# Optimization experiments

Measured on AMD Instinct MI355X. Metric: run time of the kernel, lower is better.

Reference implementation:

```python
import jax, jax.numpy as jnp
import numpy as np

CHANNELS = 512
NUM_HEADS = 8
NUM_GROUPS = 32
EPS = 1e-5


def setup_inputs() -> dict:
    key = jax.random.key(0)
    ks = jax.random.split(key, 6)
    c = CHANNELS
    x = jax.random.normal(ks[0], (8, c, 32, 32), dtype=jnp.float32)
    norm_w = jnp.ones((c,), jnp.float32)
    norm_b = jnp.zeros((c,), jnp.float32)
    # 1x1 conv1d weights stored as [out, in]
    qkv_w = jax.random.normal(ks[1], (3 * c, c), jnp.float32) * (1.0 / np.sqrt(c))
    qkv_b = jax.random.normal(ks[2], (3 * c,), jnp.float32) * 0.02
    # proj_out is zero-initialized in the original; use small random values so the
    # residual branch is exercised numerically (init values are not part of the math).
    proj_w = jax.random.normal(ks[3], (c, c), jnp.float32) * 0.02
    proj_b = jax.random.normal(ks[4], (c,), jnp.float32) * 0.02
    return {"x": x, "norm_w": norm_w, "norm_b": norm_b,
            "qkv_w": qkv_w, "qkv_b": qkv_b, "proj_w": proj_w, "proj_b": proj_b}


def _group_norm(x, w, b):
    # x: [B, C, L]; normalize per (batch, group) over (C/G, L) in float32
    B, C, L = x.shape
    xg = x.astype(jnp.float32).reshape(B, NUM_GROUPS, (C // NUM_GROUPS) * L)
    mean = xg.mean(axis=-1, keepdims=True)
    var = xg.var(axis=-1, keepdims=True)
    xn = ((xg - mean) * jax.lax.rsqrt(var + EPS)).reshape(B, C, L)
    return (xn * w[None, :, None] + b[None, :, None]).astype(x.dtype)


def _attention_legacy(qkv, n_heads):
    # qkv: [B, 3*C, L]  (QKVAttentionLegacy: split heads after reshape)
    B, width, L = qkv.shape
    ch = width // (3 * n_heads)
    q, k, v = jnp.split(qkv.reshape(B * n_heads, 3 * ch, L), 3, axis=1)
    scale = 1.0 / np.sqrt(np.sqrt(ch))
    w = jnp.einsum('bct,bcs->bts', q * scale, k * scale)  # [B*H, L, L]
    w = jax.nn.softmax(w.astype(jnp.float32), axis=-1).astype(qkv.dtype)
    a = jnp.einsum('bts,bcs->bct', w, v)  # [B*H, ch, L]
    return a.reshape(B, n_heads * ch, L)


def reference(x, norm_w, norm_b, qkv_w, qkv_b, proj_w, proj_b):
    b, c = x.shape[0], x.shape[1]
    spatial = x.shape[2:]
    x_ = x.reshape(b, c, -1)  # [B, C, L]
    xn = _group_norm(x_, norm_w, norm_b)
    qkv = jnp.einsum('oc,bcl->bol', qkv_w, xn) + qkv_b[None, :, None]
    h = _attention_legacy(qkv, NUM_HEADS)
    h = jnp.einsum('oc,bcl->bol', proj_w, h) + proj_b[None, :, None]
    return (x_ + h).reshape(b, c, *spatial)
```

## Files before the change

### kernel.cpp

```cpp
#include <hip/hip_runtime.h>
#include <hip/hip_bf16.h>
#include <stdint.h>


#define NB 8
#define NC 512
#define NL 1024
#define NHD 8
#define ND 64

typedef __attribute__((ext_vector_type(4))) float f32x4;
typedef __attribute__((ext_vector_type(8))) short bf16x8;
typedef __attribute__((ext_vector_type(4))) short bf16x4;
typedef __attribute__((ext_vector_type(4))) unsigned short u16x4;
typedef __attribute__((ext_vector_type(8))) unsigned short u16x8;

#define MFMA16(a, b, c) __builtin_amdgcn_mfma_f32_16x16x32_bf16((a), (b), (c), 0, 0, 0)

static __device__ __forceinline__ f32x4 mfma_k16(bf16x4 a, bf16x4 b, f32x4 c) {
#if __has_builtin(__builtin_amdgcn_mfma_f32_16x16x16bf16_1k)
  return __builtin_amdgcn_mfma_f32_16x16x16bf16_1k(a, b, c, 0, 0, 0);
#else
  asm("v_mfma_f32_16x16x16_bf16 %0, %1, %2, %0" : "+v"(c) : "v"(a), "v"(b));
  return c;
#endif
}

#if __has_builtin(__builtin_amdgcn_exp2f)
#define EXP2F __builtin_amdgcn_exp2f
#else
#define EXP2F exp2f
#endif

static __device__ __forceinline__ unsigned short f2bf(float f) {
  union { float f; uint32_t u; } v; v.f = f;
  uint32_t r = v.u + 0x7fffu + ((v.u >> 16) & 1u);
  return (unsigned short)(r >> 16);
}

static __device__ __forceinline__ short f2bf_h(float f) {
  __hip_bfloat16 h = __float2bfloat16(f);
  return *reinterpret_cast<short*>(&h);
}

static __device__ __forceinline__ void gl_lds16(const unsigned short* g, unsigned short* l) {
  __builtin_amdgcn_global_load_lds(
      (const __attribute__((address_space(1))) void*)g,
      (__attribute__((address_space(3))) void*)l, 16, 0, 0);
}

__global__ __launch_bounds__(256) void k_conv_w(const float* __restrict__ qkvw,
                                                const float* __restrict__ pw,
                                                unsigned short* __restrict__ qwb,
                                                unsigned short* __restrict__ pwb) {
  int i = blockIdx.x * 256 + threadIdx.x;
  const int NQ4 = (3 * NC * NC) / 4;
  if (i < NQ4) {
    f32x4 v = ((const f32x4*)qkvw)[i];
    u16x4 o; o.x = f2bf(v.x); o.y = f2bf(v.y); o.z = f2bf(v.z); o.w = f2bf(v.w);
    ((u16x4*)qwb)[i] = o;
  } else {
    int j = i - NQ4;
    f32x4 v = ((const f32x4*)pw)[j];
    u16x4 o; o.x = f2bf(v.x); o.y = f2bf(v.y); o.z = f2bf(v.z); o.w = f2bf(v.w);
    ((u16x4*)pwb)[j] = o;
  }
}

__global__ __launch_bounds__(256) void k_gnorm(const float* __restrict__ x,
                                               const float* __restrict__ nw,
                                               const float* __restrict__ nb,
                                               unsigned short* __restrict__ xnt) {
  const int b = blockIdx.x >> 5, g = blockIdx.x & 31;
  const float* base = x + ((size_t)b * NC + g * 16) * NL;
  const int t = threadIdx.x;
  f32x4 vals[16];
  float s = 0.f, ss = 0.f;
#pragma unroll
  for (int r = 0; r < 16; ++r) {
    f32x4 v = ((const f32x4*)base)[t + 256 * r];
    vals[r] = v;
    s += v.x + v.y + v.z + v.w;
    ss += v.x * v.x + v.y * v.y + v.z * v.z + v.w * v.w;
  }
#pragma unroll
  for (int m = 1; m < 64; m <<= 1) { s += __shfl_xor(s, m, 64); ss += __shfl_xor(ss, m, 64); }
  __shared__ float red[8];
  const int w = t >> 6;
  if ((t & 63) == 0) { red[w] = s; red[4 + w] = ss; }
  __syncthreads();
  s  = red[0] + red[1] + red[2] + red[3];
  ss = red[4] + red[5] + red[6] + red[7];
  const float mean = s * (1.f / 16384.f);
  const float var  = ss * (1.f / 16384.f) - mean * mean;
  const float inv  = rsqrtf(var + 1e-5f);
  u16x8 ov[4][2];
#pragma unroll
  for (int r = 0; r < 16; ++r) {
    float wcv = nw[g * 16 + r] * inv;
    float bcv = nb[g * 16 + r] - mean * wcv;
    f32x4 v = vals[r];
    ov[0][r >> 3][r & 7] = f2bf(v.x * wcv + bcv);
    ov[1][r >> 3][r & 7] = f2bf(v.y * wcv + bcv);
    ov[2][r >> 3][r & 7] = f2bf(v.z * wcv + bcv);
    ov[3][r >> 3][r & 7] = f2bf(v.w * wcv + bcv);
  }
#pragma unroll
  for (int j = 0; j < 4; ++j) {
    size_t off = ((size_t)b * NL + 4 * t + j) * NC + g * 16;
    *(u16x8*)(xnt + off)     = ov[j][0];
    *(u16x8*)(xnt + off + 8) = ov[j][1];
  }
}

__global__ __launch_bounds__(256) void k_qkv(const unsigned short* __restrict__ xnt,
                                             const unsigned short* __restrict__ qwb,
                                             const float* __restrict__ qkvb,
                                             unsigned short* __restrict__ qt,
                                             unsigned short* __restrict__ kt,
                                             unsigned short* __restrict__ vt) {
  __shared__ __align__(16) unsigned short As[128 * 64];
  __shared__ __align__(16) unsigned short Bs[128 * 64];
  const int m0 = blockIdx.x * 128;
  const int n0 = blockIdx.y * 128;
  const int b = blockIdx.z;
  const int tid = threadIdx.x, lane = tid & 63, w = tid >> 6;
  const int wr = w >> 1, wc = w & 1;

  int soff[4];
#pragma unroll
  for (int r = 0; r < 4; ++r) {
    int c = (r * 4 + w) * 64 + lane;
    int row = c >> 3, lc = (c & 7) ^ (row & 7);
    soff[r] = row * NC + lc * 8;
  }
  const unsigned short* Ap = xnt + (size_t)b * NL * NC + (size_t)m0 * NC;
  const unsigned short* Bp = qwb + (size_t)n0 * NC;

  f32x4 acc[4][4];
#pragma unroll
  for (int mi = 0; mi < 4; ++mi)
#pragma unroll
    for (int ni = 0; ni < 4; ++ni) acc[mi][ni] = (f32x4){0.f, 0.f, 0.f, 0.f};

  for (int k0 = 0; k0 < NC; k0 += 64) {
#pragma unroll
    for (int r = 0; r < 4; ++r) gl_lds16(Ap + soff[r], &As[(r * 4 + w) * 512]);
#pragma unroll
    for (int r = 0; r < 4; ++r) gl_lds16(Bp + soff[r], &Bs[(r * 4 + w) * 512]);
    Ap += 64; Bp += 64;
    __syncthreads();
#pragma unroll
    for (int ks = 0; ks < 2; ++ks) {
      bf16x8 af[4], bfr[4];
#pragma unroll
      for (int mi = 0; mi < 4; ++mi) {
        int row = wr * 64 + mi * 16 + (lane & 15);
        int ph = ((lane >> 4) + ks * 4) ^ (row & 7);
        af[mi] = *(const bf16x8*)&As[row * 64 + ph * 8];
      }
#pragma unroll
      for (int ni = 0; ni < 4; ++ni) {
        int row = wc * 64 + ni * 16 + (lane & 15);
        int ph = ((lane >> 4) + ks * 4) ^ (row & 7);
        bfr[ni] = *(const bf16x8*)&Bs[row * 64 + ph * 8];
      }
#pragma unroll
      for (int mi = 0; mi < 4; ++mi)
#pragma unroll
        for (int ni = 0; ni < 4; ++ni)
          acc[mi][ni] = MFMA16(af[mi], bfr[ni], acc[mi][ni]);
    }
    __syncthreads();
  }
#pragma unroll
  for (int ni = 0; ni < 4; ++ni) {
    int o = n0 + wc * 64 + ni * 16 + (lane & 15);
    int head = o / 192, rem = o - head * 192;
    int type = rem >> 6, ch = rem & 63;
    float bias = qkvb[o];
#pragma unroll
    for (int mi = 0; mi < 4; ++mi) {
      int l0 = m0 + wr * 64 + mi * 16 + ((lane >> 4) << 2);
      if (type == 2) {
        u16x4 pk;
#pragma unroll
        for (int i = 0; i < 4; ++i) pk[i] = f2bf(acc[mi][ni][i] + bias);
        *(u16x4*)&vt[(((size_t)(b * NHD + head) * 256 + (l0 >> 2)) * ND + ch) * 4] = pk;
      } else {
        const float sc = (type == 0)
            ? (0.35355339059327373f * 1.4426950408889634f)
            : 0.35355339059327373f;
        unsigned short* dst =
            (type == 0 ? qt : kt) + ((size_t)(b * NHD + head) * NL + l0) * ND + ch;
#pragma unroll
        for (int i = 0; i < 4; ++i)
          dst[i * ND] = f2bf((acc[mi][ni][i] + bias) * sc);
      }
    }
  }
}

__global__ __launch_bounds__(256) void k_attn(const unsigned short* __restrict__ qt,
                                              const unsigned short* __restrict__ kt,
                                              const unsigned short* __restrict__ vt,
                                              unsigned short* __restrict__ abuf) {
  __shared__ __align__(16) unsigned short Ks[2][64 * 64];
  __shared__ __align__(16) unsigned short Vs[2][64 * 64];
  const int bid = blockIdx.x;
  const int bh = (bid & 7) * 8 + (bid >> 7);
  const int tb = (bid >> 3) & 15;
  const int tid = threadIdx.x, lane = tid & 63, w = tid >> 6;
  const int lo = lane & 15, g = lane >> 4;
  const int t0 = tb * 64 + w * 16;
  const unsigned short* qb = qt + (size_t)bh * NL * ND;

  int koff[2], voff[2];
#pragma unroll
  for (int r = 0; r < 2; ++r) {
    int c = (r * 4 + w) * 64 + lane;
    int row = c >> 3, lc = (c & 7) ^ (row & 7);
    koff[r] = row * ND + lc * 8;
    voff[r] = c * 8;
  }
  const int e0 = lo * 64 + ((g ^ (lo & 7)) * 8);
  const int e1 = lo * 64 + (((4 + g) ^ (lo & 7)) * 8);
  const int vbase = g * 256 + lo * 4;

  const unsigned short* kst = kt + (size_t)bh * NL * ND;
  const unsigned short* vst = vt + (size_t)bh * NL * ND;

  bf16x8 qf[2];
#pragma unroll
  for (int ks = 0; ks < 2; ++ks)
    qf[ks] = *(const bf16x8*)&qb[(size_t)(t0 + lo) * ND + ks * 32 + g * 8];

  f32x4 pv[4];
#pragma unroll
  for (int ci = 0; ci < 4; ++ci) pv[ci] = (f32x4){0.f, 0.f, 0.f, 0.f};
  float l = 0.f;

  gl_lds16(kst + koff[0], &Ks[0][w * 512]);
  gl_lds16(kst + koff[1], &Ks[0][(4 + w) * 512]);
  gl_lds16(vst + voff[0], &Vs[0][w * 512]);
  gl_lds16(vst + voff[1], &Vs[0][(4 + w) * 512]);
  kst += 4096; vst += 4096;

#define ATTN_TILE(BUF, LAST)                                                  \
  {                                                                           \
    __syncthreads();                                                          \
    if (!(LAST)) {                                                            \
      gl_lds16(kst + koff[0], &Ks[(BUF) ^ 1][w * 512]);                       \
      gl_lds16(kst + koff[1], &Ks[(BUF) ^ 1][(4 + w) * 512]);                 \
      gl_lds16(vst + voff[0], &Vs[(BUF) ^ 1][w * 512]);                       \
      gl_lds16(vst + voff[1], &Vs[(BUF) ^ 1][(4 + w) * 512]);                 \
      kst += 4096; vst += 4096;                                               \
    }                                                                         \
    f32x4 sacc[4];                                                            \
    _Pragma("unroll")                                                         \
    for (int sblk = 0; sblk < 4; ++sblk) sacc[sblk] = (f32x4){0.f,0.f,0.f,0.f};\
    __builtin_amdgcn_s_setprio(1);                                            \
    _Pragma("unroll")                                                         \
    for (int sblk = 0; sblk < 4; ++sblk) {                                    \
      bf16x8 kf = *(const bf16x8*)&Ks[BUF][sblk * 1024 + e0];                 \
      sacc[sblk] = MFMA16(kf, qf[0], sacc[sblk]);                             \
    }                                                                         \
    _Pragma("unroll")                                                         \
    for (int sblk = 0; sblk < 4; ++sblk) {                                    \
      bf16x8 kf = *(const bf16x8*)&Ks[BUF][sblk * 1024 + e1];                 \
      sacc[sblk] = MFMA16(kf, qf[1], sacc[sblk]);                             \
    }                                                                         \
    __builtin_amdgcn_s_setprio(0);                                            \
    _Pragma("unroll")                                                         \
    for (int sblk = 0; sblk < 4; ++sblk) {                                    \
      float p0 = EXP2F(fminf(sacc[sblk][0], 80.f));                           \
      float p1 = EXP2F(fminf(sacc[sblk][1], 80.f));                           \
      float p2 = EXP2F(fminf(sacc[sblk][2], 80.f));                           \
      float p3 = EXP2F(fminf(sacc[sblk][3], 80.f));                           \
      l += (p0 + p1) + (p2 + p3);                                             \
      bf16x4 pf;                                                              \
      pf[0] = f2bf_h(p0); pf[1] = f2bf_h(p1);                                 \
      pf[2] = f2bf_h(p2); pf[3] = f2bf_h(p3);                                 \
      _Pragma("unroll")                                                       \
      for (int ci = 0; ci < 4; ++ci) {                                        \
        bf16x4 vf = *(const bf16x4*)&Vs[BUF][sblk * 1024 + ci * 64 + vbase];  \
        pv[ci] = mfma_k16(pf, vf, pv[ci]);                                    \
      }                                                                       \
    }                                                                         \
  }

  for (int it = 0; it < 16; it += 2) {
    ATTN_TILE(0, false);
    ATTN_TILE(1, it == 14);
  }
#undef ATTN_TILE

  l += __shfl_xor(l, 16);
  l += __shfl_xor(l, 32);
  float li[4];
#pragma unroll
  for (int i = 0; i < 4; ++i) li[i] = 1.0f / __shfl(l, g * 4 + i, 16);
#pragma unroll
  for (int ci = 0; ci < 4; ++ci)
#pragma unroll
    for (int i = 0; i < 4; ++i) {
      int tl = tb * 64 + w * 16 + g * 4 + i;
      abuf[((size_t)bh * NL + tl) * ND + ci * 16 + lo] = f2bf_h(pv[ci][i] * li[i]);
    }
}

__global__ __launch_bounds__(256) void k_proj(const unsigned short* __restrict__ abuf,
                                              const unsigned short* __restrict__ pwb,
                                              const float* __restrict__ pb,
                                              const float* __restrict__ x,
                                              float* __restrict__ out) {
  __shared__ __align__(16) unsigned short As[128 * 64];
  __shared__ __align__(16) unsigned short Bs[128 * 64];
  const int m0 = blockIdx.x * 128;
  const int n0 = blockIdx.y * 128;
  const int b = blockIdx.z;
  const int tid = threadIdx.x, lane = tid & 63, w = tid >> 6;
  const int wr = w >> 1, wc = w & 1;

  int aoff[4], boff[4];
#pragma unroll
  for (int r = 0; r < 4; ++r) {
    int c = (r * 4 + w) * 64 + lane;
    int row = c >> 3, lc = (c & 7) ^ (row & 7);
    aoff[r] = row * NC + lc * 8;
    boff[r] = row * ND + lc * 8;
  }
  const unsigned short* Ap = pwb + (size_t)m0 * NC;
  const unsigned short* Bp = abuf + ((size_t)(b * NHD) * NL + n0) * ND;

  f32x4 acc[4][4];
#pragma unroll
  for (int mi = 0; mi < 4; ++mi)
#pragma unroll
    for (int ni = 0; ni < 4; ++ni) acc[mi][ni] = (f32x4){0.f, 0.f, 0.f, 0.f};

  for (int k0 = 0; k0 < NC; k0 += 64) {
#pragma unroll
    for (int r = 0; r < 4; ++r) gl_lds16(Ap + aoff[r], &As[(r * 4 + w) * 512]);
#pragma unroll
    for (int r = 0; r < 4; ++r) gl_lds16(Bp + boff[r], &Bs[(r * 4 + w) * 512]);
    Ap += 64; Bp += (size_t)NL * ND;
    __syncthreads();
#pragma unroll
    for (int ks = 0; ks < 2; ++ks) {
      bf16x8 af[4], bfr[4];
#pragma unroll
      for (int mi = 0; mi < 4; ++mi) {
        int row = wr * 64 + mi * 16 + (lane & 15);
        int ph = ((lane >> 4) + ks * 4) ^ (row & 7);
        af[mi] = *(const bf16x8*)&As[row * 64 + ph * 8];
      }
#pragma unroll
      for (int ni = 0; ni < 4; ++ni) {
        int row = wc * 64 + ni * 16 + (lane & 15);
        int ph = ((lane >> 4) + ks * 4) ^ (row & 7);
        bfr[ni] = *(const bf16x8*)&Bs[row * 64 + ph * 8];
      }
#pragma unroll
      for (int mi = 0; mi < 4; ++mi)
#pragma unroll
        for (int ni = 0; ni < 4; ++ni)
          acc[mi][ni] = MFMA16(af[mi], bfr[ni], acc[mi][ni]);
    }
    __syncthreads();
  }
#pragma unroll
  for (int mi = 0; mi < 4; ++mi)
#pragma unroll
    for (int i = 0; i < 4; ++i) {
      int o = m0 + wr * 64 + mi * 16 + ((lane >> 4) << 2) + i;
      float pbv = pb[o];
#pragma unroll
      for (int ni = 0; ni < 4; ++ni) {
        int l = n0 + wc * 64 + ni * 16 + (lane & 15);
        size_t idx = ((size_t)b * NC + o) * NL + l;
        out[idx] = x[idx] + acc[mi][ni][i] + pbv;
      }
    }
}

extern "C" void kernel_launch(void* const* d_in, const int* in_sizes, int n_in,
                              void* d_out, int out_size, void* d_ws, size_t ws_size,
                              hipStream_t stream) {
  const float* x    = (const float*)d_in[0];
  const float* nw   = (const float*)d_in[1];
  const float* nb   = (const float*)d_in[2];
  const float* qkvw = (const float*)d_in[3];
  const float* qkvb = (const float*)d_in[4];
  const float* pw   = (const float*)d_in[5];
  const float* pb   = (const float*)d_in[6];
  float* out = (float*)d_out;

  char* ws = (char*)d_ws;
  unsigned short* xnt  = (unsigned short*)(ws);
  unsigned short* abuf = (unsigned short*)(ws);
  unsigned short* qwb  = (unsigned short*)(ws + 8388608);
  unsigned short* pwb  = (unsigned short*)(ws + 9961472);
  unsigned short* qt   = (unsigned short*)(ws + 10485760);
  unsigned short* kt   = (unsigned short*)(ws + 18874368);
  unsigned short* vt   = (unsigned short*)(ws + 27262976);

  k_conv_w<<<1024, 256, 0, stream>>>(qkvw, pw, qwb, pwb);
  k_gnorm<<<256, 256, 0, stream>>>(x, nw, nb, xnt);
  k_qkv<<<dim3(8, 12, 8), 256, 0, stream>>>(xnt, qwb, qkvb, qt, kt, vt);
  k_attn<<<1024, 256, 0, stream>>>(qt, kt, vt, abuf);
  k_proj<<<dim3(4, 8, 8), 256, 0, stream>>>(abuf, pwb, pb, x, out);
}
```

Baseline: 88.76 us.

## Process two query tiles per wave in attention and shrink proj M-tile

Result: slower. 92.96 us (+4.7%).

```diff
diff --git a/kernel.cpp b/kernel.cpp
--- a/kernel.cpp
+++ b/kernel.cpp
@@ -208,11 +208,11 @@
   __shared__ __align__(16) unsigned short Ks[2][64 * 64];
   __shared__ __align__(16) unsigned short Vs[2][64 * 64];
   const int bid = blockIdx.x;
-  const int bh = (bid & 7) * 8 + (bid >> 7);
-  const int tb = (bid >> 3) & 15;
+  const int bh = (bid & 7) * 8 + (bid >> 6);
+  const int tb = (bid >> 3) & 7;
   const int tid = threadIdx.x, lane = tid & 63, w = tid >> 6;
   const int lo = lane & 15, g = lane >> 4;
-  const int t0 = tb * 64 + w * 16;
+  const int t0 = tb * 128 + w * 32;
   const unsigned short* qb = qt + (size_t)bh * NL * ND;
 
   int koff[2], voff[2];
@@ -230,15 +230,19 @@
   const unsigned short* kst = kt + (size_t)bh * NL * ND;
   const unsigned short* vst = vt + (size_t)bh * NL * ND;
 
-  bf16x8 qf[2];
-#pragma unroll
-  for (int ks = 0; ks < 2; ++ks)
-    qf[ks] = *(const bf16x8*)&qb[(size_t)(t0 + lo) * ND + ks * 32 + g * 8];
-
-  f32x4 pv[4];
-#pragma unroll
-  for (int ci = 0; ci < 4; ++ci) pv[ci] = (f32x4){0.f, 0.f, 0.f, 0.f};
-  float l = 0.f;
+  bf16x8 qf[2][2];
+#pragma unroll
+  for (int h = 0; h < 2; ++h)
+#pragma unroll
+    for (int ks = 0; ks < 2; ++ks)
+      qf[h][ks] = *(const bf16x8*)&qb[(size_t)(t0 + h * 16 + lo) * ND + ks * 32 + g * 8];
+
+  f32x4 pv[2][4];
+#pragma unroll
+  for (int h = 0; h < 2; ++h)
+#pragma unroll
+    for (int ci = 0; ci < 4; ++ci) pv[h][ci] = (f32x4){0.f, 0.f, 0.f, 0.f};
+  float lsum0 = 0.f, lsum1 = 0.f;
 
   gl_lds16(kst + koff[0], &Ks[0][w * 512]);
   gl_lds16(kst + koff[1], &Ks[0][(4 + w) * 512]);
@@ -256,35 +260,49 @@
       gl_lds16(vst + voff[1], &Vs[(BUF) ^ 1][(4 + w) * 512]);                 \
       kst += 4096; vst += 4096;                                               \
     }                                                                         \
-    f32x4 sacc[4];                                                            \
+    f32x4 sacc[2][4];                                                         \
     _Pragma("unroll")                                                         \
-    for (int sblk = 0; sblk < 4; ++sblk) sacc[sblk] = (f32x4){0.f,0.f,0.f,0.f};\
+    for (int h = 0; h < 2; ++h)                                               \
+      _Pragma("unroll")                                                       \
+      for (int sblk = 0; sblk < 4; ++sblk)                                    \
+        sacc[h][sblk] = (f32x4){0.f, 0.f, 0.f, 0.f};                          \
     __builtin_amdgcn_s_setprio(1);                                            \
     _Pragma("unroll")                                                         \
     for (int sblk = 0; sblk < 4; ++sblk) {                                    \
       bf16x8 kf = *(const bf16x8*)&Ks[BUF][sblk * 1024 + e0];                 \
-      sacc[sblk] = MFMA16(kf, qf[0], sacc[sblk]);                             \
+      sacc[0][sblk] = MFMA16(kf, qf[0][0], sacc[0][sblk]);                    \
+      sacc[1][sblk] = MFMA16(kf, qf[1][0], sacc[1][sblk]);                    \
     }                                                                         \
     _Pragma("unroll")                                                         \
     for (int sblk = 0; sblk < 4; ++sblk) {                                    \
       bf16x8 kf = *(const bf16x8*)&Ks[BUF][sblk * 1024 + e1];                 \
-      sacc[sblk] = MFMA16(kf, qf[1], sacc[sblk]);                             \
+      sacc[0][sblk] = MFMA16(kf, qf[0][1], sacc[0][sblk]);                    \
+      sacc[1][sblk] = MFMA16(kf, qf[1][1], sacc[1][sblk]);                    \
     }                                                                         \
     __builtin_amdgcn_s_setprio(0);                                            \
     _Pragma("unroll")                                                         \
     for (int sblk = 0; sblk < 4; ++sblk) {                                    \
-      float p0 = EXP2F(fminf(sacc[sblk][0], 80.f));                           \
-      float p1 = EXP2F(fminf(sacc[sblk][1], 80.f));                           \
-      float p2 = EXP2F(fminf(sacc[sblk][2], 80.f));                           \
-      float p3 = EXP2F(fminf(sacc[sblk][3], 80.f));                           \
-      l += (p0 + p1) + (p2 + p3);                                             \
-      bf16x4 pf;                                                              \
-      pf[0] = f2bf_h(p0); pf[1] = f2bf_h(p1);                                 \
-      pf[2] = f2bf_h(p2); pf[3] = f2bf_h(p3);                                 \
+      float a0 = EXP2F(fminf(sacc[0][sblk][0], 80.f));                        \
+      float a1 = EXP2F(fminf(sacc[0][sblk][1], 80.f));                        \
+      float a2 = EXP2F(fminf(sacc[0][sblk][2], 80.f));                        \
+      float a3 = EXP2F(fminf(sacc[0][sblk][3], 80.f));                        \
+      lsum0 += (a0 + a1) + (a2 + a3);                                         \
+      bf16x4 pf0;                                                             \
+      pf0[0] = f2bf_h(a0); pf0[1] = f2bf_h(a1);                               \
+      pf0[2] = f2bf_h(a2); pf0[3] = f2bf_h(a3);                               \
+      float b0 = EXP2F(fminf(sacc[1][sblk][0], 80.f));                        \
+      float b1 = EXP2F(fminf(sacc[1][sblk][1], 80.f));                        \
+      float b2 = EXP2F(fminf(sacc[1][sblk][2], 80.f));                        \
+      float b3 = EXP2F(fminf(sacc[1][sblk][3], 80.f));                        \
+      lsum1 += (b0 + b1) + (b2 + b3);                                         \
+      bf16x4 pf1;                                                             \
+      pf1[0] = f2bf_h(b0); pf1[1] = f2bf_h(b1);                               \
+      pf1[2] = f2bf_h(b2); pf1[3] = f2bf_h(b3);                               \
       _Pragma("unroll")                                                       \
       for (int ci = 0; ci < 4; ++ci) {                                        \
         bf16x4 vf = *(const bf16x4*)&Vs[BUF][sblk * 1024 + ci * 64 + vbase];  \
-        pv[ci] = mfma_k16(pf, vf, pv[ci]);                                    \
+        pv[0][ci] = mfma_k16(pf0, vf, pv[0][ci]);                             \
+        pv[1][ci] = mfma_k16(pf1, vf, pv[1][ci]);                             \
       }                                                                       \
     }                                                                         \
   }
@@ -295,18 +313,22 @@
   }
 #undef ATTN_TILE
 
-  l += __shfl_xor(l, 16);
-  l += __shfl_xor(l, 32);
-  float li[4];
-#pragma unroll
-  for (int i = 0; i < 4; ++i) li[i] = 1.0f / __shfl(l, g * 4 + i, 16);
-#pragma unroll
-  for (int ci = 0; ci < 4; ++ci)
-#pragma unroll
-    for (int i = 0; i < 4; ++i) {
-      int tl = tb * 64 + w * 16 + g * 4 + i;
-      abuf[((size_t)bh * NL + tl) * ND + ci * 16 + lo] = f2bf_h(pv[ci][i] * li[i]);
-    }
+#pragma unroll
+  for (int h = 0; h < 2; ++h) {
+    float l = h ? lsum1 : lsum0;
+    l += __shfl_xor(l, 16);
+    l += __shfl_xor(l, 32);
+    float li[4];
+#pragma unroll
+    for (int i = 0; i < 4; ++i) li[i] = 1.0f / __shfl(l, g * 4 + i, 16);
+#pragma unroll
+    for (int ci = 0; ci < 4; ++ci)
+#pragma unroll
+      for (int i = 0; i < 4; ++i) {
+        int tl = t0 + h * 16 + g * 4 + i;
+        abuf[((size_t)bh * NL + tl) * ND + ci * 16 + lo] = f2bf_h(pv[h][ci][i] * li[i]);
+      }
+  }
 }
 
 __global__ __launch_bounds__(256) void k_proj(const unsigned short* __restrict__ abuf,
@@ -314,57 +336,57 @@
                                               const float* __restrict__ pb,
                                               const float* __restrict__ x,
                                               float* __restrict__ out) {
-  __shared__ __align__(16) unsigned short As[128 * 64];
+  __shared__ __align__(16) unsigned short As[64 * 64];
   __shared__ __align__(16) unsigned short Bs[128 * 64];
-  const int m0 = blockIdx.x * 128;
+  const int m0 = blockIdx.x * 64;
   const int n0 = blockIdx.y * 128;
   const int b = blockIdx.z;
   const int tid = threadIdx.x, lane = tid & 63, w = tid >> 6;
-  const int wr = w >> 1, wc = w & 1;
-
-  int aoff[4], boff[4];
+  const int lo = lane & 15, g = lane >> 4;
+
+  int aoff[2], boff[4];
 #pragma unroll
   for (int r = 0; r < 4; ++r) {
     int c = (r * 4 + w) * 64 + lane;
     int row = c >> 3, lc = (c & 7) ^ (row & 7);
-    aoff[r] = row * NC + lc * 8;
     boff[r] = row * ND + lc * 8;
+    if (r < 2) aoff[r] = row * NC + lc * 8;
   }
   const unsigned short* Ap = pwb + (size_t)m0 * NC;
   const unsigned short* Bp = abuf + ((size_t)(b * NHD) * NL + n0) * ND;
 
-  f32x4 acc[4][4];
+  f32x4 acc[4][2];
 #pragma unroll
   for (int mi = 0; mi < 4; ++mi)
 #pragma unroll
-    for (int ni = 0; ni < 4; ++ni) acc[mi][ni] = (f32x4){0.f, 0.f, 0.f, 0.f};
+    for (int ni = 0; ni < 2; ++ni) acc[mi][ni] = (f32x4){0.f, 0.f, 0.f, 0.f};
 
   for (int k0 = 0; k0 < NC; k0 += 64) {
 #pragma unroll
-    for (int r = 0; r < 4; ++r) gl_lds16(Ap + aoff[r], &As[(r * 4 + w) * 512]);
+    for (int r = 0; r < 2; ++r) gl_lds16(Ap + aoff[r], &As[(r * 4 + w) * 512]);
 #pragma unroll
     for (int r = 0; r < 4; ++r) gl_lds16(Bp + boff[r], &Bs[(r * 4 + w) * 512]);
     Ap += 64; Bp += (size_t)NL * ND;
     __syncthreads();
 #pragma unroll
     for (int ks = 0; ks < 2; ++ks) {
-      bf16x8 af[4], bfr[4];
+      bf16x8 af[4], bfr[2];
 #pragma unroll
       for (int mi = 0; mi < 4; ++mi) {
-        int row = wr * 64 + mi * 16 + (lane & 15);
-        int ph = ((lane >> 4) + ks * 4) ^ (row & 7);
+        int row = mi * 16 + lo;
+        int ph = (g + ks * 4) ^ (row & 7);
         af[mi] = *(const bf16x8*)&As[row * 64 + ph * 8];
       }
 #pragma unroll
-      for (int ni = 0; ni < 4; ++ni) {
-        int row = wc * 64 + ni * 16 + (lane & 15);
-        int ph = ((lane >> 4) + ks * 4) ^ (row & 7);
+      for (int ni = 0; ni < 2; ++ni) {
+        int row = w * 32 + ni * 16 + lo;
+        int ph = (g + ks * 4) ^ (row & 7);
         bfr[ni] = *(const bf16x8*)&Bs[row * 64 + ph * 8];
       }
 #pragma unroll
       for (int mi = 0; mi < 4; ++mi)
 #pragma unroll
-        for (int ni = 0; ni < 4; ++ni)
+        for (int ni = 0; ni < 2; ++ni)
           acc[mi][ni] = MFMA16(af[mi], bfr[ni], acc[mi][ni]);
     }
     __syncthreads();
@@ -373,11 +395,11 @@
   for (int mi = 0; mi < 4; ++mi)
 #pragma unroll
     for (int i = 0; i < 4; ++i) {
-      int o = m0 + wr * 64 + mi * 16 + ((lane >> 4) << 2) + i;
+      int o = m0 + mi * 16 + g * 4 + i;
       float pbv = pb[o];
 #pragma unroll
-      for (int ni = 0; ni < 4; ++ni) {
-        int l = n0 + wc * 64 + ni * 16 + (lane & 15);
+      for (int ni = 0; ni < 2; ++ni) {
+        int l = n0 + w * 32 + ni * 16 + lo;
         size_t idx = ((size_t)b * NC + o) * NL + l;
         out[idx] = x[idx] + acc[mi][ni][i] + pbv;
       }
@@ -408,6 +430,6 @@
   k_conv_w<<<1024, 256, 0, stream>>>(qkvw, pw, qwb, pwb);
   k_gnorm<<<256, 256, 0, stream>>>(x, nw, nb, xnt);
   k_qkv<<<dim3(8, 12, 8), 256, 0, stream>>>(xnt, qwb, qkvb, qt, kt, vt);
-  k_attn<<<1024, 256, 0, stream>>>(qt, kt, vt, abuf);
-  k_proj<<<dim3(4, 8, 8), 256, 0, stream>>>(abuf, pwb, pb, x, out);
-}
+  k_attn<<<512, 256, 0, stream>>>(qt, kt, vt, abuf);
+  k_proj<<<dim3(8, 8, 8), 256, 0, stream>>>(abuf, pwb, pb, x, out);
+}
```

## Double-buffer LDS tiles with K=32 steps in QKV and projection GEMMs

Applied to the files above, without the earlier changes.

After: 94.32 us. 6.3% more time.

```diff
diff --git a/kernel.cpp b/kernel.cpp
--- a/kernel.cpp
+++ b/kernel.cpp
@@ -119,21 +119,24 @@
                                              unsigned short* __restrict__ qt,
                                              unsigned short* __restrict__ kt,
                                              unsigned short* __restrict__ vt) {
-  __shared__ __align__(16) unsigned short As[128 * 64];
-  __shared__ __align__(16) unsigned short Bs[128 * 64];
+  __shared__ __align__(16) unsigned short As[2][128 * 32];
+  __shared__ __align__(16) unsigned short Bs[2][128 * 32];
   const int m0 = blockIdx.x * 128;
   const int n0 = blockIdx.y * 128;
   const int b = blockIdx.z;
   const int tid = threadIdx.x, lane = tid & 63, w = tid >> 6;
   const int wr = w >> 1, wc = w & 1;
-
-  int soff[4];
-#pragma unroll
-  for (int r = 0; r < 4; ++r) {
-    int c = (r * 4 + w) * 64 + lane;
-    int row = c >> 3, lc = (c & 7) ^ (row & 7);
+  const int lo = lane & 15, g = lane >> 4;
+
+  int soff[2];
+#pragma unroll
+  for (int r = 0; r < 2; ++r) {
+    int c = r * 256 + tid;
+    int row = c >> 2, lc = (c & 3) ^ ((row >> 1) & 3);
     soff[r] = row * NC + lc * 8;
   }
+  const int rph = (g ^ ((lo >> 1) & 3)) * 8;
+
   const unsigned short* Ap = xnt + (size_t)b * NL * NC + (size_t)m0 * NC;
   const unsigned short* Bp = qwb + (size_t)n0 * NC;
 
@@ -143,45 +146,55 @@
 #pragma unroll
     for (int ni = 0; ni < 4; ++ni) acc[mi][ni] = (f32x4){0.f, 0.f, 0.f, 0.f};
 
-  for (int k0 = 0; k0 < NC; k0 += 64) {
-#pragma unroll
-    for (int r = 0; r < 4; ++r) gl_lds16(Ap + soff[r], &As[(r * 4 + w) * 512]);
-#pragma unroll
-    for (int r = 0; r < 4; ++r) gl_lds16(Bp + soff[r], &Bs[(r * 4 + w) * 512]);
-    Ap += 64; Bp += 64;
-    __syncthreads();
-#pragma unroll
-    for (int ks = 0; ks < 2; ++ks) {
-      bf16x8 af[4], bfr[4];
-#pragma unroll
-      for (int mi = 0; mi < 4; ++mi) {
-        int row = wr * 64 + mi * 16 + (lane & 15);
-        int ph = ((lane >> 4) + ks * 4) ^ (row & 7);
-        af[mi] = *(const bf16x8*)&As[row * 64 + ph * 8];
-      }
-#pragma unroll
-      for (int ni = 0; ni < 4; ++ni) {
-        int row = wc * 64 + ni * 16 + (lane & 15);
-        int ph = ((lane >> 4) + ks * 4) ^ (row & 7);
-        bfr[ni] = *(const bf16x8*)&Bs[row * 64 + ph * 8];
-      }
-#pragma unroll
-      for (int mi = 0; mi < 4; ++mi)
-#pragma unroll
-        for (int ni = 0; ni < 4; ++ni)
-          acc[mi][ni] = MFMA16(af[mi], bfr[ni], acc[mi][ni]);
-    }
-    __syncthreads();
-  }
+  gl_lds16(Ap + soff[0], &As[0][w * 512]);
+  gl_lds16(Ap + soff[1], &As[0][(4 + w) * 512]);
+  gl_lds16(Bp + soff[0], &Bs[0][w * 512]);
+  gl_lds16(Bp + soff[1], &Bs[0][(4 + w) * 512]);
+  Ap += 32; Bp += 32;
+
+#define QKV_STEP(BUF, LAST)                                                   \
+  {                                                                           \
+    __syncthreads();                                                          \
+    if (!(LAST)) {                                                            \
+      gl_lds16(Ap + soff[0], &As[(BUF) ^ 1][w * 512]);                        \
+      gl_lds16(Ap + soff[1], &As[(BUF) ^ 1][(4 + w) * 512]);                  \
+      gl_lds16(Bp + soff[0], &Bs[(BUF) ^ 1][w * 512]);                        \
+      gl_lds16(Bp + soff[1], &Bs[(BUF) ^ 1][(4 + w) * 512]);                  \
+      Ap += 32; Bp += 32;                                                     \
+    }                                                                         \
+    bf16x8 af[4], bfr[4];                                                     \
+    _Pragma("unroll")                                                         \
+    for (int mi = 0; mi < 4; ++mi) {                                          \
+      int row = wr * 64 + mi * 16 + lo;                                       \
+      af[mi] = *(const bf16x8*)&As[BUF][row * 32 + rph];                      \
+    }                                                                         \
+    _Pragma("unroll")                                                         \
+    for (int ni = 0; ni < 4; ++ni) {                                          \
+      int row = wc * 64 + ni * 16 + lo;                                       \
+      bfr[ni] = *(const bf16x8*)&Bs[BUF][row * 32 + rph];                     \
+    }                                                                         \
+    _Pragma("unroll")                                                         \
+    for (int mi = 0; mi < 4; ++mi)                                            \
+      _Pragma("unroll")                                                       \
+      for (int ni = 0; ni < 4; ++ni)                                          \
+        acc[mi][ni] = MFMA16(af[mi], bfr[ni], acc[mi][ni]);                   \
+  }
+
+  for (int it = 0; it < 16; it += 2) {
+    QKV_STEP(0, false);
+    QKV_STEP(1, it == 14);
+  }
+#undef QKV_STEP
+
 #pragma unroll
   for (int ni = 0; ni < 4; ++ni) {
-    int o = n0 + wc * 64 + ni * 16 + (lane & 15);
+    int o = n0 + wc * 64 + ni * 16 + lo;
     int head = o / 192, rem = o - head * 192;
     int type = rem >> 6, ch = rem & 63;
     float bias = qkvb[o];
 #pragma unroll
     for (int mi = 0; mi < 4; ++mi) {
-      int l0 = m0 + wr * 64 + mi * 16 + ((lane >> 4) << 2);
+      int l0 = m0 + wr * 64 + mi * 16 + (g << 2);
       if (type == 2) {
         u16x4 pk;
 #pragma unroll
@@ -314,24 +327,27 @@
                                               const float* __restrict__ pb,
                                               const float* __restrict__ x,
                                               float* __restrict__ out) {
-  __shared__ __align__(16) unsigned short As[128 * 64];
-  __shared__ __align__(16) unsigned short Bs[128 * 64];
+  __shared__ __align__(16) unsigned short As[2][128 * 32];
+  __shared__ __align__(16) unsigned short Bs[2][128 * 32];
   const int m0 = blockIdx.x * 128;
   const int n0 = blockIdx.y * 128;
   const int b = blockIdx.z;
   const int tid = threadIdx.x, lane = tid & 63, w = tid >> 6;
   const int wr = w >> 1, wc = w & 1;
-
-  int aoff[4], boff[4];
-#pragma unroll
-  for (int r = 0; r < 4; ++r) {
-    int c = (r * 4 + w) * 64 + lane;
-    int row = c >> 3, lc = (c & 7) ^ (row & 7);
+  const int lo = lane & 15, g = lane >> 4;
+
+  int aoff[2], boff[2];
+#pragma unroll
+  for (int r = 0; r < 2; ++r) {
+    int c = r * 256 + tid;
+    int row = c >> 2, lc = (c & 3) ^ ((row >> 1) & 3);
     aoff[r] = row * NC + lc * 8;
     boff[r] = row * ND + lc * 8;
   }
+  const int rph = (g ^ ((lo >> 1) & 3)) * 8;
+
   const unsigned short* Ap = pwb + (size_t)m0 * NC;
-  const unsigned short* Bp = abuf + ((size_t)(b * NHD) * NL + n0) * ND;
+  const unsigned short* Bb = abuf + ((size_t)(b * NHD) * NL + n0) * ND;
 
   f32x4 acc[4][4];
 #pragma unroll
@@ -339,45 +355,57 @@
 #pragma unroll
     for (int ni = 0; ni < 4; ++ni) acc[mi][ni] = (f32x4){0.f, 0.f, 0.f, 0.f};
 
-  for (int k0 = 0; k0 < NC; k0 += 64) {
-#pragma unroll
-    for (int r = 0; r < 4; ++r) gl_lds16(Ap + aoff[r], &As[(r * 4 + w) * 512]);
-#pragma unroll
-    for (int r = 0; r < 4; ++r) gl_lds16(Bp + boff[r], &Bs[(r * 4 + w) * 512]);
-    Ap += 64; Bp += (size_t)NL * ND;
-    __syncthreads();
-#pragma unroll
-    for (int ks = 0; ks < 2; ++ks) {
-      bf16x8 af[4], bfr[4];
-#pragma unroll
-      for (int mi = 0; mi < 4; ++mi) {
-        int row = wr * 64 + mi * 16 + (lane & 15);
-        int ph = ((lane >> 4) + ks * 4) ^ (row & 7);
-        af[mi] = *(const bf16x8*)&As[row * 64 + ph * 8];
-      }
+  gl_lds16(Ap + aoff[0], &As[0][w * 512]);
+  gl_lds16(Ap + aoff[1], &As[0][(4 + w) * 512]);
+  gl_lds16(Bb + boff[0], &Bs[0][w * 512]);
+  gl_lds16(Bb + boff[1], &Bs[0][(4 + w) * 512]);
+  Ap += 32;
+
+#define PROJ_STEP(BUF, NEXTJ, LAST)                                           \
+  {                                                                           \
+    __syncthreads();                                                          \
+    if (!(LAST)) {                                                            \
+      const unsigned short* Bpj =                                             \
+          Bb + (size_t)((NEXTJ) >> 1) * (NL * ND) + ((NEXTJ) & 1) * 32;       \
+      gl_lds16(Ap + aoff[0], &As[(BUF) ^ 1][w * 512]);                        \
+      gl_lds16(Ap + aoff[1], &As[(BUF) ^ 1][(4 + w) * 512]);                  \
+      gl_lds16(Bpj + boff[0], &Bs[(BUF) ^ 1][w * 512]);                       \
+      gl_lds16(Bpj + boff[1], &Bs[(BUF) ^ 1][(4 + w) * 512]);                 \
+      Ap += 32;                                                               \
+    }                                                                         \
+    bf16x8 af[4], bfr[4];                                                     \
+    _Pragma("unroll")                                                         \
+    for (int mi = 0; mi < 4; ++mi) {                                          \
+      int row = wr * 64 + mi * 16 + lo;                                       \
+      af[mi] = *(const bf16x8*)&As[BUF][row * 32 + rph];                      \
+    }                                                                         \
+    _Pragma("unroll")                                                         \
+    for (int ni = 0; ni < 4; ++ni) {                                          \
+      int row = wc * 64 + ni * 16 + lo;                                       \
+      bfr[ni] = *(const bf16x8*)&Bs[BUF][row * 32 + rph];                     \
+    }                                                                         \
+    _Pragma("unroll")                                                         \
+    for (int mi = 0; mi < 4; ++mi)                                            \
+      _Pragma("unroll")                                                       \
+      for (int ni = 0; ni < 4; ++ni)                                          \
+        acc[mi][ni] = MFMA16(af[mi], bfr[ni], acc[mi][ni]);                   \
+  }
+
+  for (int it = 0; it < 16; it += 2) {
+    PROJ_STEP(0, it + 1, false);
+    PROJ_STEP(1, it + 2, it == 14);
+  }
+#undef PROJ_STEP
+
+#pragma unroll
+  for (int mi = 0; mi < 4; ++mi)
+#pragma unroll
+    for (int i = 0; i < 4; ++i) {
+      int o = m0 + wr * 64 + mi * 16 + g * 4 + i;
+      float pbv = pb[o];
 #pragma unroll
       for (int ni = 0; ni < 4; ++ni) {
-        int row = wc * 64 + ni * 16 + (lane & 15);
-        int ph = ((lane >> 4) + ks * 4) ^ (row & 7);
-        bfr[ni] = *(const bf16x8*)&Bs[row * 64 + ph * 8];
-      }
-#pragma unroll
-      for (int mi = 0; mi < 4; ++mi)
-#pragma unroll
-        for (int ni = 0; ni < 4; ++ni)
-          acc[mi][ni] = MFMA16(af[mi], bfr[ni], acc[mi][ni]);
-    }
-    __syncthreads();
-  }
-#pragma unroll
-  for (int mi = 0; mi < 4; ++mi)
-#pragma unroll
-    for (int i = 0; i < 4; ++i) {
-      int o = m0 + wr * 64 + mi * 16 + ((lane >> 4) << 2) + i;
-      float pbv = pb[o];
-#pragma unroll
-      for (int ni = 0; ni < 4; ++ni) {
-        int l = n0 + wc * 64 + ni * 16 + (lane & 15);
+        int l = n0 + wc * 64 + ni * 16 + lo;
         size_t idx = ((size_t)b * NC + o) * NL + l;
         out[idx] = x[idx] + acc[mi][ni][i] + pbv;
       }
```
